# Kernel optimization log

Measured on AMD Instinct MI355X. Metric: run time of the kernel, lower is better.

The kernel has to match this reference:

```python
import jax, jax.numpy as jnp
import numpy as np

PATCH = 14
MERGE = 2
HIDDEN = 1024
# (H, W) in pixels; all multiples of PATCH with even patch grids (divisible by MERGE)
IMAGE_SIZES = np.array([[1540, 1540], [1120, 1540], [1540, 896], [784, 1260],
                        [1512, 1512], [1540, 1120], [896, 896], [1260, 1540]], dtype=np.int64)


def setup_inputs() -> dict:
    key = jax.random.key(0)
    k1, k2 = jax.random.split(key)
    sizes_p = IMAGE_SIZES // PATCH
    total_tokens = int((sizes_p[:, 0] * sizes_p[:, 1]).sum())  # 67440
    image_features = jax.random.normal(k1, (total_tokens, HIDDEN), dtype=jnp.float32)
    # nn.Linear(hidden*merge**2 -> hidden, bias=False): weight shape [out, in] = [1024, 4096]
    merging_weight = jax.random.normal(k2, (HIDDEN, HIDDEN * MERGE * MERGE), dtype=jnp.float32) * 0.02
    image_sizes = jnp.asarray(IMAGE_SIZES)
    return {"image_features": image_features, "merging_weight": merging_weight, "image_sizes": image_sizes}


def _merge_patches(feats, sizes_np):
    """Per-image unfold(kernel=MERGE, stride=MERGE) over the [hp, wp] patch grid.
    torch unfold orders the flattened channel dim as d*m*m + ki*m + kj (channel-major),
    blocks in row-major (i, j) order -> reshape/transpose below reproduces it exactly."""
    m = MERGE
    D = feats.shape[-1]
    out, off = [], 0
    for h, w in sizes_np:  # small fixed set of images (static shapes)
        hp, wp = int(h) // PATCH, int(w) // PATCH
        n = hp * wp
        g = jax.lax.dynamic_slice_in_dim(feats, off, n, axis=0)
        g = g.reshape(hp // m, m, wp // m, m, D)          # [i, ki, j, kj, d]
        g = g.transpose(0, 2, 4, 1, 3).reshape(-1, D * m * m)  # [i*j, d*ki*kj]
        out.append(g)
        off += n
    return jnp.concatenate(out, axis=0)  # [total_tokens / m^2, D*m^2]


def reference(image_features, merging_weight, image_sizes):
    sizes_np = np.asarray(jax.device_get(image_sizes))  # static metadata
    merged = _merge_patches(image_features, sizes_np)
    return merged @ merging_weight.T  # [total/4, HIDDEN]
```

## Files before the change

### kernel.cpp

```cpp
#include <hip/hip_runtime.h>
#include <hip/hip_bf16.h>

#define MTOK  16860
#define NTOK  67440
#define NOUT  1024
#define KDIM  4096
#define NBM   132
#define KTILES 64

__device__ __constant__ int c_mend[8] = {3025,5225,6985,8245,11161,13361,14385,16860};
__device__ __constant__ int c_moff[8] = {0,3025,5225,6985,8245,11161,13361,14385};
__device__ __constant__ int c_foff[8] = {0,12100,20900,27940,32980,44644,53444,57540};
__device__ __constant__ int c_wp[8]   = {110,110,64,90,108,80,64,110};

typedef __attribute__((ext_vector_type(8))) short          bf16x8;
typedef __attribute__((ext_vector_type(8))) unsigned short u16x8;
typedef __attribute__((ext_vector_type(4))) float          f32x4;

#define VMCNT(n) asm volatile("s_waitcnt vmcnt(" #n ")" ::: "memory")
#define LGKM0()  asm volatile("s_waitcnt lgkmcnt(0)" ::: "memory")

__device__ __forceinline__ unsigned short f2bf(float f) {
    unsigned int u = __float_as_uint(f);
    u += 0x7FFFu + ((u >> 16) & 1u);
    return (unsigned short)(u >> 16);
}

__device__ __forceinline__ unsigned int pkbf(float lo, float hi) {
    unsigned int r;
    asm("v_cvt_pk_bf16_f32 %0, %1, %2" : "=v"(r) : "v"(lo), "v"(hi));
    return r;
}

__device__ __forceinline__ void async_copy16(const void* g, void* l) {
    __builtin_amdgcn_global_load_lds(
        (const __attribute__((address_space(1))) void*)g,
        (__attribute__((address_space(3))) void*)l, 16, 0, 0);
}

__global__ __launch_bounds__(256) void cast_w_perm(const float* __restrict__ W,
                                                   unsigned short* __restrict__ Wb) {
    int g = blockIdx.x * 256 + threadIdx.x;
    int n = g >> 10, d = g & 1023;
    float4 v = *(const float4*)(W + (size_t)n * 4096 + d * 4);
    unsigned short* o = Wb + (size_t)n * 4096 + d;
    o[0]    = f2bf(v.x);
    o[1024] = f2bf(v.y);
    o[2048] = f2bf(v.z);
    o[3072] = f2bf(v.w);
}

__global__ __launch_bounds__(256, 2) void gemm_direct(const float* __restrict__ F,
                                                      const unsigned short* __restrict__ B,
                                                      float* __restrict__ C) {
    __shared__ unsigned short lA[2][128 * 64];
    __shared__ unsigned short lB[2][128 * 64];

    const int orig    = blockIdx.y * 8 + blockIdx.x;
    const int logical = (orig & 7) * NBM + (orig >> 3);
    const int bn = logical & 7;
    const int bm = logical >> 3;

    const int tid  = threadIdx.x;
    const int wave = tid >> 6, lane = tid & 63;
    const int wm = (wave >> 1) * 64, wn = (wave & 1) * 64;

    const int srow = tid >> 3;
    const int sp   = tid & 7;
    const int sw   = srow & 7;
    const int bssw = (sp ^ sw) * 8;
    const int sdst = srow * 64 + sp * 8;

    int fbase[4], fwp[4];
#pragma unroll
    for (int i = 0; i < 4; ++i) {
        int t = bm * 128 + i * 32 + srow;
        if (t >= MTOK) t = 0;
        int im = 0;
        while (t >= c_mend[im]) im++;
        int rr  = t - c_moff[im];
        int wp  = c_wp[im];
        int wp2 = wp >> 1;
        int ii = rr / wp2, jj = rr - ii * wp2;
        fbase[i] = c_foff[im] + 2 * ii * wp + 2 * jj;
        fwp[i]   = wp;
    }
    const unsigned short* Bb = B + (size_t)(bn * 128) * KDIM;

    auto issueA = [&](int t, float4* rg) {
        const int k0 = t * 64;
        const int c  = k0 >> 10;
        const int dA = (k0 & 1023) + sp * 8;
#pragma unroll
        for (int i = 0; i < 4; ++i) {
            int fr = fbase[i] + ((c & 2) ? fwp[i] : 0) + (c & 1);
            const float* src = F + (((size_t)fr) << 10) + dA;
            rg[2 * i]     = *(const float4*)(src);
            rg[2 * i + 1] = *(const float4*)(src + 4);
        }
    };
    auto writeA = [&](float4* rg, int buf) {
#pragma unroll
        for (int i = 0; i < 4; ++i) {
            float4 x = rg[2 * i], y = rg[2 * i + 1];
            uint4 v;
            v.x = pkbf(x.x, x.y); v.y = pkbf(x.z, x.w);
            v.z = pkbf(y.x, y.y); v.w = pkbf(y.z, y.w);
            *(uint4*)&lA[buf][(i * 32 + srow) * 64 + ((sp ^ sw) * 8)] = v;
        }
    };
    auto issueB = [&](int t, int buf) {
        const int k0 = t * 64;
#pragma unroll
        for (int i = 0; i < 4; ++i)
            async_copy16(Bb + (size_t)(i * 32 + srow) * KDIM + k0 + bssw,
                         &lB[buf][i * 2048 + sdst]);
    };

    f32x4 acc[4][4];
#pragma unroll
    for (int a = 0; a < 4; ++a)
#pragma unroll
        for (int b = 0; b < 4; ++b) acc[a][b] = (f32x4){0.f, 0.f, 0.f, 0.f};

    const int mrow = lane & 15;
    const int q8   = (lane >> 4) * 8;
    const int rsw  = (mrow & 7) * 8;

    auto frag_mfma = [&](int cur) {
        bf16x8 af[2][4], bfr[2][4];
#pragma unroll
        for (int ks = 0; ks < 2; ++ks) {
            const int col = (ks * 32 + q8) ^ rsw;
#pragma unroll
            for (int a = 0; a < 4; ++a) {
                af[ks][a]  = *(const bf16x8*)&lA[cur][(wm + a * 16 + mrow) * 64 + col];
                bfr[ks][a] = *(const bf16x8*)&lB[cur][(wn + a * 16 + mrow) * 64 + col];
            }
        }
        __builtin_amdgcn_s_setprio(1);
#pragma unroll
        for (int ks = 0; ks < 2; ++ks)
#pragma unroll
            for (int a = 0; a < 4; ++a)
#pragma unroll
                for (int b = 0; b < 4; ++b)
                    acc[a][b] = __builtin_amdgcn_mfma_f32_16x16x32_bf16(af[ks][a], bfr[ks][b],
                                                                        acc[a][b], 0, 0, 0);
        __builtin_amdgcn_s_setprio(0);
    };

    float4 r1[8], r2[8];

    issueA(0, r1);
    issueB(0, 0);
    VMCNT(4);
    writeA(r1, 0);
    issueA(1, r2);
    VMCNT(8);
    LGKM0();
    __builtin_amdgcn_sched_barrier(0);
    __builtin_amdgcn_s_barrier();
    issueB(1, 1);

#pragma unroll 1
    for (int kt = 0; kt < 62; kt += 2) {
        frag_mfma(0);
        VMCNT(4);
        writeA(r2, 1);
        issueA(kt + 2, r1);
        VMCNT(8);
        LGKM0();
        __builtin_amdgcn_sched_barrier(0);
        __builtin_amdgcn_s_barrier();
        issueB(kt + 2, 0);

        frag_mfma(1);
        VMCNT(4);
        writeA(r1, 0);
        issueA(kt + 3, r2);
        VMCNT(8);
        LGKM0();
        __builtin_amdgcn_sched_barrier(0);
        __builtin_amdgcn_s_barrier();
        issueB(kt + 3, 1);
    }

    frag_mfma(0);
    VMCNT(4);
    writeA(r2, 1);
    VMCNT(0);
    LGKM0();
    __builtin_amdgcn_sched_barrier(0);
    __builtin_amdgcn_s_barrier();
    frag_mfma(1);

    const int col   = lane & 15;
    const int rquad = (lane >> 4) * 4;
#pragma unroll
    for (int a = 0; a < 4; ++a) {
        int gm0 = bm * 128 + wm + a * 16 + rquad;
#pragma unroll
        for (int b = 0; b < 4; ++b) {
            int gn = bn * 128 + wn + b * 16 + col;
#pragma unroll
            for (int rg = 0; rg < 4; ++rg) {
                int gm = gm0 + rg;
                if (gm < MTOK) C[(size_t)gm * NOUT + gn] = acc[a][b][rg];
            }
        }
    }
}

__global__ __launch_bounds__(256) void naive_fb(const float* __restrict__ feats,
                                                const float* __restrict__ W,
                                                float* __restrict__ out) {
    int t = blockIdx.x;
    int o = blockIdx.y * 256 + threadIdx.x;
    int im = 0;
    while (t >= c_mend[im]) im++;
    int r = t - c_moff[im];
    int wp = c_wp[im], wp2 = wp >> 1;
    int i = r / wp2, j = r - i * wp2;
    const float* f00 = feats + (size_t)(c_foff[im] + (2*i)*wp + 2*j) * 1024;
    const float* f10 = f00 + (size_t)wp * 1024;
    const float* w = W + (size_t)o * 4096;
    float s = 0.f;
    for (int d = 0; d < 1024; ++d)
        s += f00[d] * w[d*4] + f00[d+1024] * w[d*4+1] + f10[d] * w[d*4+2] + f10[d+1024] * w[d*4+3];
    out[(size_t)t * 1024 + o] = s;
}

extern "C" void kernel_launch(void* const* d_in, const int* in_sizes, int n_in,
                              void* d_out, int out_size, void* d_ws, size_t ws_size,
                              hipStream_t stream) {
    const float* feats = (const float*)d_in[0];
    const float* W     = (const float*)d_in[1];
    float* out         = (float*)d_out;

    const size_t need = (size_t)NOUT * KDIM * sizeof(unsigned short);
    if (ws_size >= need) {
        unsigned short* Wb = (unsigned short*)d_ws;
        cast_w_perm<<<dim3(4096), 256, 0, stream>>>(W, Wb);
        gemm_direct<<<dim3(8, NBM), 256, 0, stream>>>(feats, Wb, out);
    } else {
        naive_fb<<<dim3(MTOK, 4), 256, 0, stream>>>(feats, W, out);
    }
}
```

Measured before the change: 604.3 us.

## Deepen A-prefetch to two tiles ahead and split MFMA phase into halves

Restructures the GEMM main loop so global loads of A are issued two k-tiles ahead, at the start of each phase, instead of right after the LDS write. The MFMA work is split into two k-halves, with the A conversion and LDS write placed between them, so memory latency and LDS writes overlap with matrix math. This needs more A registers live at once, and the reworked vmcnt counts must exactly match the outstanding loads for the data to be correct.

```diff
diff --git a/kernel.cpp b/kernel.cpp
--- a/kernel.cpp
+++ b/kernel.cpp
@@ -87,7 +87,7 @@
     }
     const unsigned short* Bb = B + (size_t)(bn * 128) * KDIM;
 
-    auto issueA = [&](int t, float4* rg) {
+    auto issueA = [&](int t, float4 (&rg)[8]) {
         const int k0 = t * 64;
         const int c  = k0 >> 10;
         const int dA = (k0 & 1023) + sp * 8;
@@ -99,7 +99,7 @@
             rg[2 * i + 1] = *(const float4*)(src + 4);
         }
     };
-    auto writeA = [&](float4* rg, int buf) {
+    auto writeA = [&](float4 (&rg)[8], int buf) {
 #pragma unroll
         for (int i = 0; i < 4; ++i) {
             float4 x = rg[2 * i], y = rg[2 * i + 1];
@@ -125,75 +125,89 @@
 
     const int mrow = lane & 15;
     const int q8   = (lane >> 4) * 8;
-    const int rsw  = (mrow & 7) * 8;
-
-    auto frag_mfma = [&](int cur) {
-        bf16x8 af[2][4], bfr[2][4];
-#pragma unroll
-        for (int ks = 0; ks < 2; ++ks) {
-            const int col = (ks * 32 + q8) ^ rsw;
-#pragma unroll
-            for (int a = 0; a < 4; ++a) {
-                af[ks][a]  = *(const bf16x8*)&lA[cur][(wm + a * 16 + mrow) * 64 + col];
-                bfr[ks][a] = *(const bf16x8*)&lB[cur][(wn + a * 16 + mrow) * 64 + col];
-            }
-        }
+    const int rsw  = (mrow & 15 & 7) * 8;
+
+    auto reads_half = [&](int cur, int ks, bf16x8 (&af)[4], bf16x8 (&bf_)[4]) {
+        const int col = (ks * 32 + q8) ^ rsw;
+#pragma unroll
+        for (int a = 0; a < 4; ++a) {
+            af[a]  = *(const bf16x8*)&lA[cur][(wm + a * 16 + mrow) * 64 + col];
+            bf_[a] = *(const bf16x8*)&lB[cur][(wn + a * 16 + mrow) * 64 + col];
+        }
+    };
+    auto mfma_half = [&](bf16x8 (&af)[4], bf16x8 (&bf_)[4]) {
         __builtin_amdgcn_s_setprio(1);
 #pragma unroll
-        for (int ks = 0; ks < 2; ++ks)
-#pragma unroll
-            for (int a = 0; a < 4; ++a)
-#pragma unroll
-                for (int b = 0; b < 4; ++b)
-                    acc[a][b] = __builtin_amdgcn_mfma_f32_16x16x32_bf16(af[ks][a], bfr[ks][b],
-                                                                        acc[a][b], 0, 0, 0);
+        for (int a = 0; a < 4; ++a)
+#pragma unroll
+            for (int b = 0; b < 4; ++b)
+                acc[a][b] = __builtin_amdgcn_mfma_f32_16x16x32_bf16(af[a], bf_[b],
+                                                                    acc[a][b], 0, 0, 0);
         __builtin_amdgcn_s_setprio(0);
     };
 
-    float4 r1[8], r2[8];
-
-    issueA(0, r1);
+    float4 rT0[8], rT1[8];
+
+    issueA(0, rT0);
     issueB(0, 0);
-    VMCNT(4);
-    writeA(r1, 0);
-    issueA(1, r2);
+    issueA(1, rT1);
+    VMCNT(12);
+    writeA(rT0, 0);
     VMCNT(8);
     LGKM0();
     __builtin_amdgcn_sched_barrier(0);
     __builtin_amdgcn_s_barrier();
+    __builtin_amdgcn_sched_barrier(0);
     issueB(1, 1);
+
+    auto phase_steady = [&](int cur, float4 (&rIss)[8], float4 (&rWr)[8], int ktNext) {
+        issueA(ktNext, rIss);
+        bf16x8 a0[4], b0[4];
+        reads_half(cur, 0, a0, b0);
+        mfma_half(a0, b0);
+        VMCNT(12);
+        bf16x8 a1[4], b1[4];
+        reads_half(cur, 1, a1, b1);
+        writeA(rWr, cur ^ 1);
+        __builtin_amdgcn_sched_barrier(0);
+        mfma_half(a1, b1);
+        VMCNT(8);
+        LGKM0();
+        __builtin_amdgcn_sched_barrier(0);
+        __builtin_amdgcn_s_barrier();
+        __builtin_amdgcn_sched_barrier(0);
+        issueB(ktNext, cur);
+    };
 
 #pragma unroll 1
     for (int kt = 0; kt < 62; kt += 2) {
-        frag_mfma(0);
+        phase_steady(0, rT0, rT1, kt + 2);
+        phase_steady(1, rT1, rT0, kt + 3);
+    }
+
+    {
+        bf16x8 a0[4], b0[4];
+        reads_half(0, 0, a0, b0);
+        mfma_half(a0, b0);
         VMCNT(4);
-        writeA(r2, 1);
-        issueA(kt + 2, r1);
-        VMCNT(8);
+        bf16x8 a1[4], b1[4];
+        reads_half(0, 1, a1, b1);
+        writeA(rT1, 1);
+        __builtin_amdgcn_sched_barrier(0);
+        mfma_half(a1, b1);
+        VMCNT(0);
         LGKM0();
         __builtin_amdgcn_sched_barrier(0);
         __builtin_amdgcn_s_barrier();
-        issueB(kt + 2, 0);
-
-        frag_mfma(1);
-        VMCNT(4);
-        writeA(r1, 0);
-        issueA(kt + 3, r2);
-        VMCNT(8);
-        LGKM0();
-        __builtin_amdgcn_sched_barrier(0);
-        __builtin_amdgcn_s_barrier();
-        issueB(kt + 3, 1);
-    }
-
-    frag_mfma(0);
-    VMCNT(4);
-    writeA(r2, 1);
-    VMCNT(0);
-    LGKM0();
-    __builtin_amdgcn_sched_barrier(0);
-    __builtin_amdgcn_s_barrier();
-    frag_mfma(1);
+    }
+    {
+        bf16x8 a0[4], b0[4];
+        reads_half(1, 0, a0, b0);
+        mfma_half(a0, b0);
+        bf16x8 a1[4], b1[4];
+        reads_half(1, 1, a1, b1);
+        mfma_half(a1, b1);
+    }
 
     const int col   = lane & 15;
     const int rquad = (lane >> 4) * 4;
```

New measurement: 590.8 us. 2.2% less time.

## Use 8-wave 256x128 GEMM tiles with interleaved half-step fragment pipelining

Applied to the files above, without the earlier changes.

The fused gather+GEMM moves from 4 waves on a 128x128 tile to 8 waves on a 256x128 tile, which halves the number of M blocks. Each k-tile is now split into two halves: LDS fragment reads, global A loads and async B copies are interleaved with MFMA halves under extra barriers and scheduling fences. The aim is to reuse each B tile across more rows and to hide load latency behind MFMA work. The costs are a larger LDS footprint, more barriers per k-tile, and fewer blocks (528) to fill the GPU.

```diff
diff --git a/kernel.cpp b/kernel.cpp
--- a/kernel.cpp
+++ b/kernel.cpp
@@ -2,10 +2,9 @@
 #include <hip/hip_bf16.h>
 
 #define MTOK  16860
-#define NTOK  67440
 #define NOUT  1024
 #define KDIM  4096
-#define NBM   132
+#define NBM   66
 #define KTILES 64
 
 __device__ __constant__ int c_mend[8] = {3025,5225,6985,8245,11161,13361,14385,16860};
@@ -14,11 +13,12 @@
 __device__ __constant__ int c_wp[8]   = {110,110,64,90,108,80,64,110};
 
 typedef __attribute__((ext_vector_type(8))) short          bf16x8;
-typedef __attribute__((ext_vector_type(8))) unsigned short u16x8;
 typedef __attribute__((ext_vector_type(4))) float          f32x4;
 
 #define VMCNT(n) asm volatile("s_waitcnt vmcnt(" #n ")" ::: "memory")
 #define LGKM0()  asm volatile("s_waitcnt lgkmcnt(0)" ::: "memory")
+#define BARR()   __builtin_amdgcn_s_barrier()
+#define SCHED0() __builtin_amdgcn_sched_barrier(0)
 
 __device__ __forceinline__ unsigned short f2bf(float f) {
     unsigned int u = __float_as_uint(f);
@@ -50,10 +50,10 @@
     o[3072] = f2bf(v.w);
 }
 
-__global__ __launch_bounds__(256, 2) void gemm_direct(const float* __restrict__ F,
-                                                      const unsigned short* __restrict__ B,
-                                                      float* __restrict__ C) {
-    __shared__ unsigned short lA[2][128 * 64];
+__global__ __launch_bounds__(512, 2) void gemm8(const float* __restrict__ F,
+                                                const unsigned short* __restrict__ B,
+                                                float* __restrict__ C) {
+    __shared__ unsigned short lA[2][256 * 64];
     __shared__ unsigned short lB[2][128 * 64];
 
     const int orig    = blockIdx.y * 8 + blockIdx.x;
@@ -63,7 +63,8 @@
 
     const int tid  = threadIdx.x;
     const int wave = tid >> 6, lane = tid & 63;
-    const int wm = (wave >> 1) * 64, wn = (wave & 1) * 64;
+    const int wmOff = (wave >> 1) * 64;
+    const int wnOff = (wave & 1) * 64;
 
     const int srow = tid >> 3;
     const int sp   = tid & 7;
@@ -74,7 +75,7 @@
     int fbase[4], fwp[4];
 #pragma unroll
     for (int i = 0; i < 4; ++i) {
-        int t = bm * 128 + i * 32 + srow;
+        int t = bm * 256 + i * 64 + srow;
         if (t >= MTOK) t = 0;
         int im = 0;
         while (t >= c_mend[im]) im++;
@@ -87,8 +88,8 @@
     }
     const unsigned short* Bb = B + (size_t)(bn * 128) * KDIM;
 
-    auto issueA = [&](int t, float4* rg) {
-        const int k0 = t * 64;
+    auto issueA = [&](int kt, float4 (&rg)[8]) {
+        const int k0 = kt * 64;
         const int c  = k0 >> 10;
         const int dA = (k0 & 1023) + sp * 8;
 #pragma unroll
@@ -99,22 +100,22 @@
             rg[2 * i + 1] = *(const float4*)(src + 4);
         }
     };
-    auto writeA = [&](float4* rg, int buf) {
+    auto writeA = [&](float4 (&rg)[8], int buf) {
 #pragma unroll
         for (int i = 0; i < 4; ++i) {
             float4 x = rg[2 * i], y = rg[2 * i + 1];
             uint4 v;
             v.x = pkbf(x.x, x.y); v.y = pkbf(x.z, x.w);
             v.z = pkbf(y.x, y.y); v.w = pkbf(y.z, y.w);
-            *(uint4*)&lA[buf][(i * 32 + srow) * 64 + ((sp ^ sw) * 8)] = v;
-        }
-    };
-    auto issueB = [&](int t, int buf) {
-        const int k0 = t * 64;
-#pragma unroll
-        for (int i = 0; i < 4; ++i)
-            async_copy16(Bb + (size_t)(i * 32 + srow) * KDIM + k0 + bssw,
-                         &lB[buf][i * 2048 + sdst]);
+            *(uint4*)&lA[buf][(i * 64 + srow) * 64 + ((sp ^ sw) * 8)] = v;
+        }
+    };
+    auto issueB = [&](int kt, int buf) {
+        const int k0 = kt * 64;
+#pragma unroll
+        for (int i = 0; i < 2; ++i)
+            async_copy16(Bb + (size_t)(i * 64 + srow) * KDIM + k0 + bssw,
+                         &lB[buf][i * 4096 + sdst]);
     };
 
     f32x4 acc[4][4];
@@ -127,82 +128,107 @@
     const int q8   = (lane >> 4) * 8;
     const int rsw  = (mrow & 7) * 8;
 
-    auto frag_mfma = [&](int cur) {
-        bf16x8 af[2][4], bfr[2][4];
+    bf16x8 af[2][2], bfr[4][2];
+    auto readFrags = [&](int buf, int h) {
 #pragma unroll
         for (int ks = 0; ks < 2; ++ks) {
             const int col = (ks * 32 + q8) ^ rsw;
 #pragma unroll
-            for (int a = 0; a < 4; ++a) {
-                af[ks][a]  = *(const bf16x8*)&lA[cur][(wm + a * 16 + mrow) * 64 + col];
-                bfr[ks][a] = *(const bf16x8*)&lB[cur][(wn + a * 16 + mrow) * 64 + col];
-            }
-        }
+            for (int ai = 0; ai < 2; ++ai)
+                af[ai][ks] = *(const bf16x8*)&lA[buf][(wmOff + (2 * h + ai) * 16 + mrow) * 64 + col];
+#pragma unroll
+            for (int b = 0; b < 4; ++b)
+                bfr[b][ks] = *(const bf16x8*)&lB[buf][(wnOff + b * 16 + mrow) * 64 + col];
+        }
+    };
+    auto mfmaHalf = [&](int h) {
         __builtin_amdgcn_s_setprio(1);
 #pragma unroll
-        for (int ks = 0; ks < 2; ++ks)
-#pragma unroll
-            for (int a = 0; a < 4; ++a)
-#pragma unroll
-                for (int b = 0; b < 4; ++b)
-                    acc[a][b] = __builtin_amdgcn_mfma_f32_16x16x32_bf16(af[ks][a], bfr[ks][b],
-                                                                        acc[a][b], 0, 0, 0);
+        for (int ai = 0; ai < 2; ++ai)
+#pragma unroll
+            for (int b = 0; b < 4; ++b)
+#pragma unroll
+                for (int ks = 0; ks < 2; ++ks)
+                    acc[2 * h + ai][b] = __builtin_amdgcn_mfma_f32_16x16x32_bf16(
+                        af[ai][ks], bfr[b][ks], acc[2 * h + ai][b], 0, 0, 0);
         __builtin_amdgcn_s_setprio(0);
     };
 
-    float4 r1[8], r2[8];
-
-    issueA(0, r1);
+    float4 rE[8], rO[8];
+
+    issueA(0, rE);
     issueB(0, 0);
-    VMCNT(4);
-    writeA(r1, 0);
-    issueA(1, r2);
+    VMCNT(2);
+    writeA(rE, 0);
+    issueA(1, rO);
     VMCNT(8);
     LGKM0();
-    __builtin_amdgcn_sched_barrier(0);
-    __builtin_amdgcn_s_barrier();
-    issueB(1, 1);
+    SCHED0();
+    BARR();
 
 #pragma unroll 1
-    for (int kt = 0; kt < 62; kt += 2) {
-        frag_mfma(0);
-        VMCNT(4);
-        writeA(r2, 1);
-        issueA(kt + 2, r1);
+    for (int j = 0; j < 31; ++j) {
+        readFrags(0, 0);
+        issueB(2 * j + 1, 1);
+        BARR(); SCHED0();
+        mfmaHalf(0);
+        SCHED0(); LGKM0(); BARR();
+        VMCNT(2);
+        writeA(rO, 1);
+        readFrags(0, 1);
+        issueA(2 * j + 2, rE);
+        BARR(); SCHED0();
+        mfmaHalf(1);
+        SCHED0();
         VMCNT(8);
-        LGKM0();
-        __builtin_amdgcn_sched_barrier(0);
-        __builtin_amdgcn_s_barrier();
-        issueB(kt + 2, 0);
-
-        frag_mfma(1);
-        VMCNT(4);
-        writeA(r1, 0);
-        issueA(kt + 3, r2);
+        LGKM0(); BARR();
+        readFrags(1, 0);
+        issueB(2 * j + 2, 0);
+        BARR(); SCHED0();
+        mfmaHalf(0);
+        SCHED0(); LGKM0(); BARR();
+        VMCNT(2);
+        writeA(rE, 0);
+        readFrags(1, 1);
+        issueA(2 * j + 3, rO);
+        BARR(); SCHED0();
+        mfmaHalf(1);
+        SCHED0();
         VMCNT(8);
-        LGKM0();
-        __builtin_amdgcn_sched_barrier(0);
-        __builtin_amdgcn_s_barrier();
-        issueB(kt + 3, 1);
-    }
-
-    frag_mfma(0);
-    VMCNT(4);
-    writeA(r2, 1);
+        LGKM0(); BARR();
+    }
+
+    readFrags(0, 0);
+    issueB(63, 1);
+    BARR(); SCHED0();
+    mfmaHalf(0);
+    SCHED0(); LGKM0(); BARR();
+
+    VMCNT(2);
+    writeA(rO, 1);
+    readFrags(0, 1);
+    BARR(); SCHED0();
+    mfmaHalf(1);
+    SCHED0();
     VMCNT(0);
-    LGKM0();
-    __builtin_amdgcn_sched_barrier(0);
-    __builtin_amdgcn_s_barrier();
-    frag_mfma(1);
+    LGKM0(); BARR();
+
+    readFrags(1, 0);
+    BARR(); SCHED0();
+    mfmaHalf(0);
+    SCHED0(); BARR();
+
+    readFrags(1, 1);
+    mfmaHalf(1);
 
     const int col   = lane & 15;
     const int rquad = (lane >> 4) * 4;
 #pragma unroll
     for (int a = 0; a < 4; ++a) {
-        int gm0 = bm * 128 + wm + a * 16 + rquad;
+        int gm0 = bm * 256 + wmOff + a * 16 + rquad;
 #pragma unroll
         for (int b = 0; b < 4; ++b) {
-            int gn = bn * 128 + wn + b * 16 + col;
+            int gn = bn * 128 + wnOff + b * 16 + col;
 #pragma unroll
             for (int rg = 0; rg < 4; ++rg) {
                 int gm = gm0 + rg;
@@ -242,7 +268,7 @@
     if (ws_size >= need) {
         unsigned short* Wb = (unsigned short*)d_ws;
         cast_w_perm<<<dim3(4096), 256, 0, stream>>>(W, Wb);
-        gemm_direct<<<dim3(8, NBM), 256, 0, stream>>>(feats, Wb, out);
+        gemm8<<<dim3(8, NBM), 512, 0, stream>>>(feats, Wb, out);
     } else {
         naive_fb<<<dim3(MTOK, 4), 256, 0, stream>>>(feats, W, out);
     }
```

Result: slower. 753.4 us (+24.7%).
